# Kernel optimization log

Measured on AMD Instinct MI355X. Metric: run time of the kernel, lower is better.

Reference implementation:

```python
import jax, jax.numpy as jnp
import numpy as np

B = 32768      # batch of ODE state evaluations
N = 64         # input_size (number of variables / per-node MLPs)
H = 64         # hidden_size
N_DISCRETE = 16  # first 16 variables use straight-through gating
HIDDEN_FLAG = True


def setup_inputs() -> dict:
    key = jax.random.key(0)
    k1, k2, k3 = jax.random.split(key, 3)
    inputs = jax.random.normal(k1, (B, N), jnp.float32)
    # Stacked per-node MLP weights: net_i is Linear(N,H,bias=False) -> ReLU -> Linear(H,1,bias=False)
    W1 = jax.random.normal(k2, (N, H, N), jnp.float32) / np.sqrt(N).astype(np.float32)
    W2 = jax.random.normal(k3, (N, H), jnp.float32) / np.sqrt(H).astype(np.float32)
    adjacency = jnp.ones((N, N), jnp.float32)  # buffer, initialized to ones
    discrete_mask = jnp.arange(N) < N_DISCRETE  # bool [N], from input_type_list
    return {"t": 0, "inputs": inputs, "W1": W1, "W2": W2,
            "adjacency": adjacency, "discrete_mask": discrete_mask}


def reference(t, inputs, W1, W2, adjacency, discrete_mask):
    # Straight-through discrete gating: y_hard - sg(y_soft) + y_soft
    y_soft = jax.nn.sigmoid(inputs)
    st = (inputs > 0).astype(inputs.dtype) - jax.lax.stop_gradient(y_soft) + y_soft
    x = jnp.where(discrete_mask[None, :], st, inputs)  # [B, N]

    # Effective per-node input mask: row i of adjacency; last node additionally
    # filtered to only its own (hidden) feature when hidden_flag is set.
    M = adjacency
    if HIDDEN_FLAG:
        one_hot_last = jnp.zeros((N,), M.dtype).at[-1].set(1.0)
        M = M.at[-1].set(M[-1] * one_hot_last)

    # Masking the input of node i by M[i] is equivalent to masking W1[i]'s input dim.
    W1m = W1 * M[:, None, :]                      # [N, H, N]
    h = jax.nn.relu(jnp.einsum('bn,ihn->bih', x, W1m))  # [B, N, H]
    out = jnp.einsum('bih,ih->bi', h, W2)               # [B, N]
    return out
```

## Files before the change

kernel.cpp:

```cpp
#include <hip/hip_runtime.h>
#include <stdint.h>


typedef __attribute__((ext_vector_type(8))) short short8;
typedef __attribute__((ext_vector_type(4))) float floatx4;

#define NN 64
#define HH 64
#define BB 32768
#define ITER 4
#define LDSW 20
#define X_ELEMS (BB * NN)
#define W1_ELEMS (NN * HH * NN)

__device__ __forceinline__ unsigned short f32_to_bf16_bits(float f) {
    union { float f; unsigned int i; } c; c.f = f;
    unsigned int b = c.i;
    b += 0x7fffu + ((b >> 16) & 1u);
    return (unsigned short)(b >> 16);
}

__device__ __forceinline__ bool sniff_bf16(const void* x) {
    const int lane = threadIdx.x & 63;
    const ushort* xw = (const ushort*)x;
    const ushort a = xw[4 * lane];
    const ushort b = xw[4 * lane + 2];
    const int ea = (a >> 7) & 0xFF, eb = (b >> 7) & 0xFF;
    const int hit = ((ea >= 118 && ea <= 132) ? 1 : 0) + ((eb >= 118 && eb <= 132) ? 1 : 0);
    const unsigned long long m1 = __ballot(hit >= 1);
    const unsigned long long m2 = __ballot(hit >= 2);
    return (__popcll(m1) + __popcll(m2)) >= 64;
}

__global__ __launch_bounds__(256, 4)
void prep_kernel(const void* __restrict__ x, const void* __restrict__ w1,
                 ushort* __restrict__ xo, ushort* __restrict__ w1o)
{
    const bool is_bf16 = sniff_bf16(x);
    const long base = ((long)blockIdx.x * 256 + (long)threadIdx.x) * 8;

    if (base < X_ELEMS) {
        const bool gate = (base & 63) < 16;
        short8 v;
        if (is_bf16) {
            v = *(const short8*)((const ushort*)x + base);
            if (gate) {
                #pragma unroll
                for (int j = 0; j < 8; ++j) {
                    const unsigned short u = (unsigned short)v[j];
                    const bool pos = ((u & 0x8000u) == 0) && ((u & 0x7fffu) != 0);
                    v[j] = pos ? (short)0x3F80 : (short)0;
                }
            }
        } else {
            const float* p = (const float*)x + base;
            const float4 f0 = *(const float4*)(p);
            const float4 f1 = *(const float4*)(p + 4);
            const float vals[8] = {f0.x, f0.y, f0.z, f0.w, f1.x, f1.y, f1.z, f1.w};
            #pragma unroll
            for (int j = 0; j < 8; ++j) {
                if (gate) v[j] = (vals[j] > 0.f) ? (short)0x3F80 : (short)0;
                else      v[j] = (short)f32_to_bf16_bits(vals[j]);
            }
        }
        *(short8*)(xo + base) = v;
    } else {
        const long wb = base - X_ELEMS;
        if (wb < W1_ELEMS) {
            short8 v;
            if (is_bf16) {
                v = *(const short8*)((const ushort*)w1 + wb);
            } else {
                const float* p = (const float*)w1 + wb;
                const float4 f0 = *(const float4*)(p);
                const float4 f1 = *(const float4*)(p + 4);
                const float vals[8] = {f0.x, f0.y, f0.z, f0.w, f1.x, f1.y, f1.z, f1.w};
                #pragma unroll
                for (int j = 0; j < 8; ++j) v[j] = (short)f32_to_bf16_bits(vals[j]);
            }
            const int node = (int)(wb >> 12);
            if (node == NN - 1) {
                const int w63 = (int)(wb & 63);
                #pragma unroll
                for (int j = 0; j < 8; ++j)
                    if (w63 + j != NN - 1) v[j] = 0;
            }
            *(short8*)(w1o + wb) = v;
        }
    }
}

template<bool F32>
__device__ __forceinline__ void main_body(const ushort* __restrict__ xo,
                                          const ushort* __restrict__ w1o,
                                          const void* __restrict__ w2p,
                                          void* __restrict__ outp,
                                          float* myLds)
{
    const int tid  = threadIdx.x;
    const int wave = tid >> 6;
    const int lane = tid & 63;
    const int quad = lane >> 4;
    const int l16  = lane & 15;

    const int blk  = blockIdx.x;
    const int ng   = blk >> 7;
    const int rbg  = blk & 127;
    const int node = ng * 4 + wave;
    const int rowbase = rbg * (ITER * 64);

    short8 bfrag[2][4];
    const ushort* w1n = w1o + node * (HH * NN);
    #pragma unroll
    for (int ks = 0; ks < 2; ++ks)
        #pragma unroll
        for (int ht = 0; ht < 4; ++ht)
            bfrag[ks][ht] = *(const short8*)(w1n + (ht * 16 + l16) * NN + ks * 32 + quad * 8);

    float w2reg[4];
    #pragma unroll
    for (int ht = 0; ht < 4; ++ht) {
        const int idx = node * HH + ht * 16 + l16;
        if (F32) {
            w2reg[ht] = ((const float*)w2p)[idx];
        } else {
            const ushort u = ((const ushort*)w2p)[idx];
            union { unsigned int i; float f; } cv; cv.i = ((unsigned int)u) << 16;
            w2reg[ht] = cv.f;
        }
    }

    #pragma unroll 1
    for (int it = 0; it < ITER; ++it) {
        const int b0 = rowbase + it * 64;

        short8 afrag[2][4];
        #pragma unroll
        for (int ks = 0; ks < 2; ++ks)
            #pragma unroll
            for (int rt = 0; rt < 4; ++rt)
                afrag[ks][rt] = *(const short8*)(xo + (b0 + rt * 16 + l16) * NN + ks * 32 + quad * 8);

        floatx4 acc[4][4];
        #pragma unroll
        for (int rt = 0; rt < 4; ++rt)
            #pragma unroll
            for (int ht = 0; ht < 4; ++ht)
                acc[rt][ht] = (floatx4){0.f, 0.f, 0.f, 0.f};

        #pragma unroll
        for (int ks = 0; ks < 2; ++ks)
            #pragma unroll
            for (int rt = 0; rt < 4; ++rt)
                #pragma unroll
                for (int ht = 0; ht < 4; ++ht)
                    acc[rt][ht] = __builtin_amdgcn_mfma_f32_16x16x32_bf16(
                        afrag[ks][rt], bfrag[ks][ht], acc[rt][ht], 0, 0, 0);

        #pragma unroll
        for (int rt = 0; rt < 4; ++rt) {
            #pragma unroll
            for (int r = 0; r < 4; ++r) {
                float s = 0.f;
                #pragma unroll
                for (int ht = 0; ht < 4; ++ht) {
                    float v = acc[rt][ht][r];
                    v = v > 0.f ? v : 0.f;
                    s = fmaf(v, w2reg[ht], s);
                }
                myLds[(rt * 16 + quad * 4 + r) * LDSW + l16] = s;
            }
        }

        const float* rowp = myLds + lane * LDSW;
        const float4 v0 = *(const float4*)(rowp + 0);
        const float4 v1 = *(const float4*)(rowp + 4);
        const float4 v2 = *(const float4*)(rowp + 8);
        const float4 v3 = *(const float4*)(rowp + 12);
        const float s0 = (v0.x + v0.y) + (v0.z + v0.w);
        const float s1 = (v1.x + v1.y) + (v1.z + v1.w);
        const float s2 = (v2.x + v2.y) + (v2.z + v2.w);
        const float s3 = (v3.x + v3.y) + (v3.z + v3.w);
        const float tot = (s0 + s1) + (s2 + s3);

        if (F32) ((float*) outp)[(size_t)(b0 + lane) * NN + node] = tot;
        else     ((ushort*)outp)[(size_t)(b0 + lane) * NN + node] = f32_to_bf16_bits(tot);
    }
}

__global__ __launch_bounds__(256, 3)
void main_kernel(const void* __restrict__ xorig,
                 const ushort* __restrict__ xo, const ushort* __restrict__ w1o,
                 const void* __restrict__ w2p, void* __restrict__ outp)
{
    __shared__ float lds[4][64 * LDSW];
    const bool is_bf16 = sniff_bf16(xorig);
    float* myLds = &lds[threadIdx.x >> 6][0];
    if (is_bf16) main_body<false>(xo, w1o, w2p, outp, myLds);
    else         main_body<true >(xo, w1o, w2p, outp, myLds);
}

template<bool F32>
__device__ __forceinline__ void run_body_fb(const void* xp, const void* w1p,
                                            const void* w2p, void* outp,
                                            float* myLds)
{
    const int tid  = threadIdx.x;
    const int wave = tid >> 6;
    const int lane = tid & 63;
    const int quad = lane >> 4;
    const int l16  = lane & 15;
    const int blk  = blockIdx.x;
    const int ng   = blk >> 7;
    const int rbg  = blk & 127;
    const int node = ng * 4 + wave;
    const int rowbase = rbg * (ITER * 64);

    short8 bfrag[2][4];
    #pragma unroll
    for (int ks = 0; ks < 2; ++ks) {
        #pragma unroll
        for (int ht = 0; ht < 4; ++ht) {
            const int h = ht * 16 + l16;
            const int k = ks * 32 + quad * 8;
            short8 v;
            if (F32) {
                const float* p = (const float*)w1p + node * (HH * NN) + h * NN + k;
                const float4 a0 = *(const float4*)(p);
                const float4 a1 = *(const float4*)(p + 4);
                const float vals[8] = {a0.x, a0.y, a0.z, a0.w, a1.x, a1.y, a1.z, a1.w};
                #pragma unroll
                for (int j = 0; j < 8; ++j) v[j] = (short)f32_to_bf16_bits(vals[j]);
            } else {
                v = *(const short8*)((const ushort*)w1p + node * (HH * NN) + h * NN + k);
            }
            if (node == NN - 1) {
                #pragma unroll
                for (int j = 0; j < 8; ++j)
                    if (k + j != NN - 1) v[j] = 0;
            }
            bfrag[ks][ht] = v;
        }
    }

    float w2reg[4];
    #pragma unroll
    for (int ht = 0; ht < 4; ++ht) {
        const int idx = node * HH + ht * 16 + l16;
        if (F32) {
            w2reg[ht] = ((const float*)w2p)[idx];
        } else {
            const ushort u = ((const ushort*)w2p)[idx];
            union { unsigned int i; float f; } cv; cv.i = ((unsigned int)u) << 16;
            w2reg[ht] = cv.f;
        }
    }

    #pragma unroll 1
    for (int it = 0; it < ITER; ++it) {
        const int b0 = rowbase + it * 64;
        short8 afrag[2][4];
        #pragma unroll
        for (int ks = 0; ks < 2; ++ks) {
            #pragma unroll
            for (int rt = 0; rt < 4; ++rt) {
                const int row = b0 + rt * 16 + l16;
                const int k   = ks * 32 + quad * 8;
                const bool gate = (ks == 0 && quad < 2);
                short8 v;
                if (F32) {
                    const float* p = (const float*)xp + row * NN + k;
                    const float4 a0 = *(const float4*)(p);
                    const float4 a1 = *(const float4*)(p + 4);
                    const float vals[8] = {a0.x, a0.y, a0.z, a0.w, a1.x, a1.y, a1.z, a1.w};
                    #pragma unroll
                    for (int j = 0; j < 8; ++j) {
                        if (gate) v[j] = (vals[j] > 0.f) ? (short)0x3F80 : (short)0;
                        else      v[j] = (short)f32_to_bf16_bits(vals[j]);
                    }
                } else {
                    v = *(const short8*)((const ushort*)xp + row * NN + k);
                    if (gate) {
                        #pragma unroll
                        for (int j = 0; j < 8; ++j) {
                            const unsigned short u = (unsigned short)v[j];
                            const bool pos = ((u & 0x8000u) == 0) && ((u & 0x7fffu) != 0);
                            v[j] = pos ? (short)0x3F80 : (short)0;
                        }
                    }
                }
                afrag[ks][rt] = v;
            }
        }

        floatx4 acc[4][4];
        #pragma unroll
        for (int rt = 0; rt < 4; ++rt)
            #pragma unroll
            for (int ht = 0; ht < 4; ++ht)
                acc[rt][ht] = (floatx4){0.f, 0.f, 0.f, 0.f};
        #pragma unroll
        for (int ks = 0; ks < 2; ++ks)
            #pragma unroll
            for (int rt = 0; rt < 4; ++rt)
                #pragma unroll
                for (int ht = 0; ht < 4; ++ht)
                    acc[rt][ht] = __builtin_amdgcn_mfma_f32_16x16x32_bf16(
                        afrag[ks][rt], bfrag[ks][ht], acc[rt][ht], 0, 0, 0);

        #pragma unroll
        for (int rt = 0; rt < 4; ++rt) {
            #pragma unroll
            for (int r = 0; r < 4; ++r) {
                float s = 0.f;
                #pragma unroll
                for (int ht = 0; ht < 4; ++ht) {
                    float v = acc[rt][ht][r];
                    v = v > 0.f ? v : 0.f;
                    s = fmaf(v, w2reg[ht], s);
                }
                myLds[(rt * 16 + quad * 4 + r) * LDSW + l16] = s;
            }
        }
        __syncthreads();
        const float* rowp = myLds + lane * LDSW;
        const float4 v0 = *(const float4*)(rowp + 0);
        const float4 v1 = *(const float4*)(rowp + 4);
        const float4 v2 = *(const float4*)(rowp + 8);
        const float4 v3 = *(const float4*)(rowp + 12);
        const float tot = (((v0.x + v0.y) + (v0.z + v0.w)) + ((v1.x + v1.y) + (v1.z + v1.w)))
                        + (((v2.x + v2.y) + (v2.z + v2.w)) + ((v3.x + v3.y) + (v3.z + v3.w)));
        if (F32) ((float*) outp)[(size_t)(b0 + lane) * NN + node] = tot;
        else     ((ushort*)outp)[(size_t)(b0 + lane) * NN + node] = f32_to_bf16_bits(tot);
        __syncthreads();
    }
}

__global__ __launch_bounds__(256, 2)
void fallback_kernel(const void* __restrict__ x, const void* __restrict__ W1,
                     const void* __restrict__ W2, void* __restrict__ out)
{
    __shared__ float lds[4][64 * LDSW];
    const bool is_bf16 = sniff_bf16(x);
    float* myLds = &lds[threadIdx.x >> 6][0];
    if (is_bf16) run_body_fb<false>(x, W1, W2, out, myLds);
    else         run_body_fb<true >(x, W1, W2, out, myLds);
}

extern "C" void kernel_launch(void* const* d_in, const int* in_sizes, int n_in,
                              void* d_out, int out_size, void* d_ws, size_t ws_size,
                              hipStream_t stream) {
    int i_in = -1, i_w1 = -1, i_w2 = -1;
    for (int i = 0; i < n_in; ++i) {
        const int s = in_sizes[i];
        if      (s == BB * NN  && i_in < 0) i_in = i;
        else if (s == NN*HH*NN && i_w1 < 0) i_w1 = i;
        else if (s == NN*HH    && i_w2 < 0) i_w2 = i;
    }
    if (i_in < 0) i_in = (n_in > 1) ? 1 : 0;
    if (i_w1 < 0) i_w1 = i_in + 1;
    if (i_w2 < 0) i_w2 = i_w1 + 1;

    const size_t need = (size_t)(X_ELEMS + W1_ELEMS) * sizeof(ushort);
    if (ws_size >= need) {
        ushort* xo  = (ushort*)d_ws;
        ushort* w1o = xo + X_ELEMS;
        prep_kernel<<<dim3((X_ELEMS + W1_ELEMS) / (256 * 8)), dim3(256), 0, stream>>>(
            d_in[i_in], d_in[i_w1], xo, w1o);
        main_kernel<<<dim3(16 * 128), dim3(256), 0, stream>>>(
            d_in[i_in], xo, w1o, d_in[i_w2], d_out);
    } else {
        fallback_kernel<<<dim3(16 * 128), dim3(256), 0, stream>>>(
            d_in[i_in], d_in[i_w1], d_in[i_w2], d_out);
    }
}
```

Before: 118.0 us.

## Swap loop order: hold x tile, iterate nodes with prefetched weights, coalesce output

Each wave now keeps one 64-row x tile in registers and loops over 4 nodes, prefetching the next node's W1 fragments while computing the current one. Before, it held one node's weights and looped over 4 row tiles. Results for 16 nodes are staged in a shared LDS tile and written as coalesced float4/ushort4 rows, replacing the scattered per-node scalar stores. This cuts strided output writes and reloads of x, at the cost of more registers (double-buffered B fragments, 16 W2 values), a block barrier, and occupancy lowered from 3 to 2 blocks per CU.

```diff
diff --git a/kernel.cpp b/kernel.cpp
--- a/kernel.cpp
+++ b/kernel.cpp
@@ -8,7 +8,6 @@
 #define NN 64
 #define HH 64
 #define BB 32768
-#define ITER 4
 #define LDSW 20
 #define X_ELEMS (BB * NN)
 #define W1_ELEMS (NN * HH * NN)
@@ -95,7 +94,7 @@
                                           const ushort* __restrict__ w1o,
                                           const void* __restrict__ w2p,
                                           void* __restrict__ outp,
-                                          float* myLds)
+                                          float* slab, float* outTile)
 {
     const int tid  = threadIdx.x;
     const int wave = tid >> 6;
@@ -104,42 +103,54 @@
     const int l16  = lane & 15;
 
     const int blk  = blockIdx.x;
-    const int ng   = blk >> 7;
-    const int rbg  = blk & 127;
-    const int node = ng * 4 + wave;
-    const int rowbase = rbg * (ITER * 64);
-
-    short8 bfrag[2][4];
-    const ushort* w1n = w1o + node * (HH * NN);
+    const int ng   = blk >> 9;
+    const int rbg  = blk & 511;
+    const int b0   = rbg * 64;
+    const int nbase = ng * 16 + wave * 4;
+
+    short8 afrag[2][4];
     #pragma unroll
     for (int ks = 0; ks < 2; ++ks)
         #pragma unroll
-        for (int ht = 0; ht < 4; ++ht)
-            bfrag[ks][ht] = *(const short8*)(w1n + (ht * 16 + l16) * NN + ks * 32 + quad * 8);
-
-    float w2reg[4];
+        for (int rt = 0; rt < 4; ++rt)
+            afrag[ks][rt] = *(const short8*)(xo + (b0 + rt * 16 + l16) * NN + ks * 32 + quad * 8);
+
+    float w2reg[4][4];
     #pragma unroll
-    for (int ht = 0; ht < 4; ++ht) {
-        const int idx = node * HH + ht * 16 + l16;
-        if (F32) {
-            w2reg[ht] = ((const float*)w2p)[idx];
-        } else {
-            const ushort u = ((const ushort*)w2p)[idx];
-            union { unsigned int i; float f; } cv; cv.i = ((unsigned int)u) << 16;
-            w2reg[ht] = cv.f;
-        }
+    for (int nl = 0; nl < 4; ++nl) {
+        #pragma unroll
+        for (int ht = 0; ht < 4; ++ht) {
+            const int idx = (nbase + nl) * HH + ht * 16 + l16;
+            if (F32) {
+                w2reg[nl][ht] = ((const float*)w2p)[idx];
+            } else {
+                const ushort u = ((const ushort*)w2p)[idx];
+                union { unsigned int i; float f; } cv; cv.i = ((unsigned int)u) << 16;
+                w2reg[nl][ht] = cv.f;
+            }
+        }
+    }
+
+    short8 bcur[2][4], bnxt[2][4];
+    {
+        const ushort* w1n = w1o + nbase * (HH * NN);
+        #pragma unroll
+        for (int ks = 0; ks < 2; ++ks)
+            #pragma unroll
+            for (int ht = 0; ht < 4; ++ht)
+                bcur[ks][ht] = *(const short8*)(w1n + (ht * 16 + l16) * NN + ks * 32 + quad * 8);
     }
 
     #pragma unroll 1
-    for (int it = 0; it < ITER; ++it) {
-        const int b0 = rowbase + it * 64;
-
-        short8 afrag[2][4];
-        #pragma unroll
-        for (int ks = 0; ks < 2; ++ks)
-            #pragma unroll
-            for (int rt = 0; rt < 4; ++rt)
-                afrag[ks][rt] = *(const short8*)(xo + (b0 + rt * 16 + l16) * NN + ks * 32 + quad * 8);
+    for (int nl = 0; nl < 4; ++nl) {
+        if (nl < 3) {
+            const ushort* w1n = w1o + (nbase + nl + 1) * (HH * NN);
+            #pragma unroll
+            for (int ks = 0; ks < 2; ++ks)
+                #pragma unroll
+                for (int ht = 0; ht < 4; ++ht)
+                    bnxt[ks][ht] = *(const short8*)(w1n + (ht * 16 + l16) * NN + ks * 32 + quad * 8);
+        }
 
         floatx4 acc[4][4];
         #pragma unroll
@@ -155,7 +166,7 @@
                 #pragma unroll
                 for (int ht = 0; ht < 4; ++ht)
                     acc[rt][ht] = __builtin_amdgcn_mfma_f32_16x16x32_bf16(
-                        afrag[ks][rt], bfrag[ks][ht], acc[rt][ht], 0, 0, 0);
+                        afrag[ks][rt], bcur[ks][ht], acc[rt][ht], 0, 0, 0);
 
         #pragma unroll
         for (int rt = 0; rt < 4; ++rt) {
@@ -166,38 +177,58 @@
                 for (int ht = 0; ht < 4; ++ht) {
                     float v = acc[rt][ht][r];
                     v = v > 0.f ? v : 0.f;
-                    s = fmaf(v, w2reg[ht], s);
+                    s = fmaf(v, w2reg[nl][ht], s);
                 }
-                myLds[(rt * 16 + quad * 4 + r) * LDSW + l16] = s;
-            }
-        }
-
-        const float* rowp = myLds + lane * LDSW;
+                slab[(rt * 16 + quad * 4 + r) * LDSW + l16] = s;
+            }
+        }
+
+        const float* rowp = slab + lane * LDSW;
         const float4 v0 = *(const float4*)(rowp + 0);
         const float4 v1 = *(const float4*)(rowp + 4);
         const float4 v2 = *(const float4*)(rowp + 8);
         const float4 v3 = *(const float4*)(rowp + 12);
-        const float s0 = (v0.x + v0.y) + (v0.z + v0.w);
-        const float s1 = (v1.x + v1.y) + (v1.z + v1.w);
-        const float s2 = (v2.x + v2.y) + (v2.z + v2.w);
-        const float s3 = (v3.x + v3.y) + (v3.z + v3.w);
-        const float tot = (s0 + s1) + (s2 + s3);
-
-        if (F32) ((float*) outp)[(size_t)(b0 + lane) * NN + node] = tot;
-        else     ((ushort*)outp)[(size_t)(b0 + lane) * NN + node] = f32_to_bf16_bits(tot);
-    }
-}
-
-__global__ __launch_bounds__(256, 3)
+        const float tot = (((v0.x + v0.y) + (v0.z + v0.w)) + ((v1.x + v1.y) + (v1.z + v1.w)))
+                        + (((v2.x + v2.y) + (v2.z + v2.w)) + ((v3.x + v3.y) + (v3.z + v3.w)));
+
+        outTile[lane * LDSW + wave * 4 + nl] = tot;
+
+        if (nl < 3) {
+            #pragma unroll
+            for (int ks = 0; ks < 2; ++ks)
+                #pragma unroll
+                for (int ht = 0; ht < 4; ++ht)
+                    bcur[ks][ht] = bnxt[ks][ht];
+        }
+    }
+
+    __syncthreads();
+
+    const int row = tid >> 2;
+    const int c   = tid & 3;
+    const float4 v = *(const float4*)(outTile + row * LDSW + c * 4);
+    const size_t obase = (size_t)(b0 + row) * NN + ng * 16 + c * 4;
+    if (F32) {
+        *(float4*)((float*)outp + obase) = v;
+    } else {
+        ushort4 o;
+        o.x = f32_to_bf16_bits(v.x); o.y = f32_to_bf16_bits(v.y);
+        o.z = f32_to_bf16_bits(v.z); o.w = f32_to_bf16_bits(v.w);
+        *(ushort4*)((ushort*)outp + obase) = o;
+    }
+}
+
+__global__ __launch_bounds__(256, 2)
 void main_kernel(const void* __restrict__ xorig,
                  const ushort* __restrict__ xo, const ushort* __restrict__ w1o,
                  const void* __restrict__ w2p, void* __restrict__ outp)
 {
-    __shared__ float lds[4][64 * LDSW];
+    __shared__ float lds[5 * 64 * LDSW];
     const bool is_bf16 = sniff_bf16(xorig);
-    float* myLds = &lds[threadIdx.x >> 6][0];
-    if (is_bf16) main_body<false>(xo, w1o, w2p, outp, myLds);
-    else         main_body<true >(xo, w1o, w2p, outp, myLds);
+    float* slab    = &lds[(threadIdx.x >> 6) * 64 * LDSW];
+    float* outTile = &lds[4 * 64 * LDSW];
+    if (is_bf16) main_body<false>(xo, w1o, w2p, outp, slab, outTile);
+    else         main_body<true >(xo, w1o, w2p, outp, slab, outTile);
 }
 
 template<bool F32>
@@ -214,7 +245,7 @@
     const int ng   = blk >> 7;
     const int rbg  = blk & 127;
     const int node = ng * 4 + wave;
-    const int rowbase = rbg * (ITER * 64);
+    const int rowbase = rbg * 256;
 
     short8 bfrag[2][4];
     #pragma unroll
@@ -257,19 +288,19 @@
     }
 
     #pragma unroll 1
-    for (int it = 0; it < ITER; ++it) {
+    for (int it = 0; it < 4; ++it) {
         const int b0 = rowbase + it * 64;
         short8 afrag[2][4];
         #pragma unroll
         for (int ks = 0; ks < 2; ++ks) {
             #pragma unroll
             for (int rt = 0; rt < 4; ++rt) {
-                const int row = b0 + rt * 16 + l16;
-                const int k   = ks * 32 + quad * 8;
+                const int rowg = b0 + rt * 16 + l16;
+                const int k    = ks * 32 + quad * 8;
                 const bool gate = (ks == 0 && quad < 2);
                 short8 v;
                 if (F32) {
-                    const float* p = (const float*)xp + row * NN + k;
+                    const float* p = (const float*)xp + rowg * NN + k;
                     const float4 a0 = *(const float4*)(p);
                     const float4 a1 = *(const float4*)(p + 4);
                     const float vals[8] = {a0.x, a0.y, a0.z, a0.w, a1.x, a1.y, a1.z, a1.w};
@@ -279,7 +310,7 @@
                         else      v[j] = (short)f32_to_bf16_bits(vals[j]);
                     }
                 } else {
-                    v = *(const short8*)((const ushort*)xp + row * NN + k);
+                    v = *(const short8*)((const ushort*)xp + rowg * NN + k);
                     if (gate) {
                         #pragma unroll
                         for (int j = 0; j < 8; ++j) {
@@ -367,7 +398,7 @@
         ushort* w1o = xo + X_ELEMS;
         prep_kernel<<<dim3((X_ELEMS + W1_ELEMS) / (256 * 8)), dim3(256), 0, stream>>>(
             d_in[i_in], d_in[i_w1], xo, w1o);
-        main_kernel<<<dim3(16 * 128), dim3(256), 0, stream>>>(
+        main_kernel<<<dim3(4 * 512), dim3(256), 0, stream>>>(
             d_in[i_in], xo, w1o, d_in[i_w2], d_out);
     } else {
         fallback_kernel<<<dim3(16 * 128), dim3(256), 0, stream>>>(
```

New measurement: 116.2 us. Within noise of the previous version (-1.5%).

## Use 16-wave blocks with LDS output tile for coalesced vector stores

Applied to the files above, without the earlier changes.

Each block now holds 16 waves, one per node, over a 32-row batch slab, and drops the 4-iteration row loop. Per-node results are gathered into a shared LDS output tile, and 128 threads write them back as contiguous float4 or ushort4 chunks. This replaces the old strided scalar stores, one element per row per node. In exchange, every wave reloads its W1 fragments for only 32 rows, so the weight fragment loads are amortised over far fewer rows. It also adds a block-wide barrier and uses 1024-thread blocks, which limits how many blocks fit on each CU.

```diff
diff --git a/kernel.cpp b/kernel.cpp
--- a/kernel.cpp
+++ b/kernel.cpp
@@ -8,7 +8,6 @@
 #define NN 64
 #define HH 64
 #define BB 32768
-#define ITER 4
 #define LDSW 20
 #define X_ELEMS (BB * NN)
 #define W1_ELEMS (NN * HH * NN)
@@ -95,7 +94,7 @@
                                           const ushort* __restrict__ w1o,
                                           const void* __restrict__ w2p,
                                           void* __restrict__ outp,
-                                          float* myLds)
+                                          float* slab, float* outTile)
 {
     const int tid  = threadIdx.x;
     const int wave = tid >> 6;
@@ -104,10 +103,10 @@
     const int l16  = lane & 15;
 
     const int blk  = blockIdx.x;
-    const int ng   = blk >> 7;
-    const int rbg  = blk & 127;
-    const int node = ng * 4 + wave;
-    const int rowbase = rbg * (ITER * 64);
+    const int ng   = blk >> 10;
+    const int rbg  = blk & 1023;
+    const int b0   = rbg * 32;
+    const int node = ng * 16 + wave;
 
     short8 bfrag[2][4];
     const ushort* w1n = w1o + node * (HH * NN);
@@ -130,74 +129,83 @@
         }
     }
 
-    #pragma unroll 1
-    for (int it = 0; it < ITER; ++it) {
-        const int b0 = rowbase + it * 64;
-
-        short8 afrag[2][4];
-        #pragma unroll
-        for (int ks = 0; ks < 2; ++ks)
-            #pragma unroll
-            for (int rt = 0; rt < 4; ++rt)
-                afrag[ks][rt] = *(const short8*)(xo + (b0 + rt * 16 + l16) * NN + ks * 32 + quad * 8);
-
-        floatx4 acc[4][4];
-        #pragma unroll
-        for (int rt = 0; rt < 4; ++rt)
+    short8 afrag[2][2];
+    #pragma unroll
+    for (int ks = 0; ks < 2; ++ks)
+        #pragma unroll
+        for (int rt = 0; rt < 2; ++rt)
+            afrag[ks][rt] = *(const short8*)(xo + (b0 + rt * 16 + l16) * NN + ks * 32 + quad * 8);
+
+    floatx4 acc[2][4];
+    #pragma unroll
+    for (int rt = 0; rt < 2; ++rt)
+        #pragma unroll
+        for (int ht = 0; ht < 4; ++ht)
+            acc[rt][ht] = (floatx4){0.f, 0.f, 0.f, 0.f};
+
+    #pragma unroll
+    for (int ks = 0; ks < 2; ++ks)
+        #pragma unroll
+        for (int rt = 0; rt < 2; ++rt)
             #pragma unroll
             for (int ht = 0; ht < 4; ++ht)
-                acc[rt][ht] = (floatx4){0.f, 0.f, 0.f, 0.f};
-
-        #pragma unroll
-        for (int ks = 0; ks < 2; ++ks)
-            #pragma unroll
-            for (int rt = 0; rt < 4; ++rt)
-                #pragma unroll
-                for (int ht = 0; ht < 4; ++ht)
-                    acc[rt][ht] = __builtin_amdgcn_mfma_f32_16x16x32_bf16(
-                        afrag[ks][rt], bfrag[ks][ht], acc[rt][ht], 0, 0, 0);
-
-        #pragma unroll
-        for (int rt = 0; rt < 4; ++rt) {
-            #pragma unroll
-            for (int r = 0; r < 4; ++r) {
-                float s = 0.f;
-                #pragma unroll
-                for (int ht = 0; ht < 4; ++ht) {
-                    float v = acc[rt][ht][r];
-                    v = v > 0.f ? v : 0.f;
-                    s = fmaf(v, w2reg[ht], s);
-                }
-                myLds[(rt * 16 + quad * 4 + r) * LDSW + l16] = s;
-            }
-        }
-
-        const float* rowp = myLds + lane * LDSW;
-        const float4 v0 = *(const float4*)(rowp + 0);
-        const float4 v1 = *(const float4*)(rowp + 4);
-        const float4 v2 = *(const float4*)(rowp + 8);
-        const float4 v3 = *(const float4*)(rowp + 12);
-        const float s0 = (v0.x + v0.y) + (v0.z + v0.w);
-        const float s1 = (v1.x + v1.y) + (v1.z + v1.w);
-        const float s2 = (v2.x + v2.y) + (v2.z + v2.w);
-        const float s3 = (v3.x + v3.y) + (v3.z + v3.w);
-        const float tot = (s0 + s1) + (s2 + s3);
-
-        if (F32) ((float*) outp)[(size_t)(b0 + lane) * NN + node] = tot;
-        else     ((ushort*)outp)[(size_t)(b0 + lane) * NN + node] = f32_to_bf16_bits(tot);
-    }
-}
-
-__global__ __launch_bounds__(256, 3)
+                acc[rt][ht] = __builtin_amdgcn_mfma_f32_16x16x32_bf16(
+                    afrag[ks][rt], bfrag[ks][ht], acc[rt][ht], 0, 0, 0);
+
+    #pragma unroll
+    for (int rt = 0; rt < 2; ++rt) {
+        #pragma unroll
+        for (int r = 0; r < 4; ++r) {
+            float s = 0.f;
+            #pragma unroll
+            for (int ht = 0; ht < 4; ++ht) {
+                float v = acc[rt][ht][r];
+                v = v > 0.f ? v : 0.f;
+                s = fmaf(v, w2reg[ht], s);
+            }
+            slab[(rt * 16 + quad * 4 + r) * LDSW + l16] = s;
+        }
+    }
+
+    const int row = lane & 31;
+    const float* rowp = slab + row * LDSW;
+    const float4 v0 = *(const float4*)(rowp + 0);
+    const float4 v1 = *(const float4*)(rowp + 4);
+    const float4 v2 = *(const float4*)(rowp + 8);
+    const float4 v3 = *(const float4*)(rowp + 12);
+    const float tot = (((v0.x + v0.y) + (v0.z + v0.w)) + ((v1.x + v1.y) + (v1.z + v1.w)))
+                    + (((v2.x + v2.y) + (v2.z + v2.w)) + ((v3.x + v3.y) + (v3.z + v3.w)));
+    if (lane < 32) outTile[row * LDSW + wave] = tot;
+
+    __syncthreads();
+
+    if (tid < 128) {
+        const int orow = tid >> 2;
+        const int c    = tid & 3;
+        const float4 v = *(const float4*)(outTile + orow * LDSW + c * 4);
+        const size_t obase = (size_t)(b0 + orow) * NN + ng * 16 + c * 4;
+        if (F32) {
+            *(float4*)((float*)outp + obase) = v;
+        } else {
+            ushort4 o;
+            o.x = f32_to_bf16_bits(v.x); o.y = f32_to_bf16_bits(v.y);
+            o.z = f32_to_bf16_bits(v.z); o.w = f32_to_bf16_bits(v.w);
+            *(ushort4*)((ushort*)outp + obase) = o;
+        }
+    }
+}
+
+__global__ __launch_bounds__(1024)
 void main_kernel(const void* __restrict__ xorig,
                  const ushort* __restrict__ xo, const ushort* __restrict__ w1o,
                  const void* __restrict__ w2p, void* __restrict__ outp)
 {
-    __shared__ float lds[4][64 * LDSW];
+    __shared__ float lds[17 * 32 * LDSW];
     const bool is_bf16 = sniff_bf16(xorig);
-    float* myLds = &lds[threadIdx.x >> 6][0];
-    if (is_bf16) main_body<false>(xo, w1o, w2p, outp, myLds);
-    else         main_body<true >(xo, w1o, w2p, outp, myLds);
+    float* slab    = &lds[(threadIdx.x >> 6) * 32 * LDSW];
+    float* outTile = &lds[16 * 32 * LDSW];
+    if (is_bf16) main_body<false>(xo, w1o, w2p, outp, slab, outTile);
+    else         main_body<true >(xo, w1o, w2p, outp, slab, outTile);
 }
 
 template<bool F32>
@@ -214,7 +222,7 @@
     const int ng   = blk >> 7;
     const int rbg  = blk & 127;
     const int node = ng * 4 + wave;
-    const int rowbase = rbg * (ITER * 64);
+    const int rowbase = rbg * 256;
 
     short8 bfrag[2][4];
     #pragma unroll
@@ -257,19 +265,19 @@
     }
 
     #pragma unroll 1
-    for (int it = 0; it < ITER; ++it) {
+    for (int it = 0; it < 4; ++it) {
         const int b0 = rowbase + it * 64;
         short8 afrag[2][4];
         #pragma unroll
         for (int ks = 0; ks < 2; ++ks) {
             #pragma unroll
             for (int rt = 0; rt < 4; ++rt) {
-                const int row = b0 + rt * 16 + l16;
-                const int k   = ks * 32 + quad * 8;
+                const int rowg = b0 + rt * 16 + l16;
+                const int k    = ks * 32 + quad * 8;
                 const bool gate = (ks == 0 && quad < 2);
                 short8 v;
                 if (F32) {
-                    const float* p = (const float*)xp + row * NN + k;
+                    const float* p = (const float*)xp + rowg * NN + k;
                     const float4 a0 = *(const float4*)(p);
                     const float4 a1 = *(const float4*)(p + 4);
                     const float vals[8] = {a0.x, a0.y, a0.z, a0.w, a1.x, a1.y, a1.z, a1.w};
@@ -279,7 +287,7 @@
                         else      v[j] = (short)f32_to_bf16_bits(vals[j]);
                     }
                 } else {
-                    v = *(const short8*)((const ushort*)xp + row * NN + k);
+                    v = *(const short8*)((const ushort*)xp + rowg * NN + k);
                     if (gate) {
                         #pragma unroll
                         for (int j = 0; j < 8; ++j) {
@@ -367,7 +375,7 @@
         ushort* w1o = xo + X_ELEMS;
         prep_kernel<<<dim3((X_ELEMS + W1_ELEMS) / (256 * 8)), dim3(256), 0, stream>>>(
             d_in[i_in], d_in[i_w1], xo, w1o);
-        main_kernel<<<dim3(16 * 128), dim3(256), 0, stream>>>(
+        main_kernel<<<dim3(4 * 1024), dim3(1024), 0, stream>>>(
             d_in[i_in], xo, w1o, d_in[i_w2], d_out);
     } else {
         fallback_kernel<<<dim3(16 * 128), dim3(256), 0, stream>>>(
```

Measured after the change: 170.9 us. 1.45x slower.
